# Performance work log

Hardware: AMD Instinct MI355X
Metric: run time of the kernel (lower is better)

The kernel has to match this reference:

```python
import jax, jax.numpy as jnp
import numpy as np


def _xavier(key, shape):
    fan_out, fan_in = shape[0], shape[1]
    lim = np.sqrt(6.0 / (fan_in + fan_out)).astype(np.float32)
    return jax.random.uniform(key, shape, jnp.float32, -lim, lim)


def setup_inputs() -> dict:
    key = jax.random.key(0)
    ks = jax.random.split(key, 28)
    B, D, G, ND = 16384, 32, 6, 8
    V_user, V_item, V_gender, V_age, V_occ, V_genre = 1000000, 100000, 2, 7, 21, 19
    H1, H2 = 128, 64
    deep_in = 6 * D + ND  # 200
    return {
        "user_id": jax.random.randint(ks[0], (B,), 0, V_user),
        "item_id": jax.random.randint(ks[1], (B,), 0, V_item),
        "user_gender": jax.random.randint(ks[2], (B,), 0, V_gender),
        "user_age": jax.random.randint(ks[3], (B,), 0, V_age),
        "user_occupation": jax.random.randint(ks[4], (B,), 0, V_occ),
        "item_genre_ids": jax.random.randint(ks[5], (B, G), 0, V_genre),
        "item_genre_mask": jax.random.randint(ks[6], (B, G), 0, 2).astype(jnp.float32),
        "dense_features": jax.random.normal(ks[7], (B, ND), jnp.float32),
        # first-order (1-dim) embedding tables
        "fo_user": _xavier(ks[8], (V_user, 1)),
        "fo_item": _xavier(ks[9], (V_item, 1)),
        "fo_gender": _xavier(ks[10], (V_gender, 1)),
        "fo_age": _xavier(ks[11], (V_age, 1)),
        "fo_occ": _xavier(ks[12], (V_occ, 1)),
        "fo_genre": _xavier(ks[13], (V_genre, 1)),
        # second-order / deep embedding tables
        "emb_user": _xavier(ks[14], (V_user, D)),
        "emb_item": _xavier(ks[15], (V_item, D)),
        "emb_gender": _xavier(ks[16], (V_gender, D)),
        "emb_age": _xavier(ks[17], (V_age, D)),
        "emb_occ": _xavier(ks[18], (V_occ, D)),
        "emb_genre": _xavier(ks[19], (V_genre, D)),
        # dense linear + deep MLP
        "dense_W": _xavier(ks[20], (1, ND)),
        "dense_b": jnp.zeros((1,), jnp.float32),
        "W1": _xavier(ks[21], (H1, deep_in)),
        "b1": jnp.zeros((H1,), jnp.float32),
        "W2": _xavier(ks[22], (H2, H1)),
        "b2": jnp.zeros((H2,), jnp.float32),
        "Wout": _xavier(ks[23], (1, H2)),
        "bout": jnp.zeros((1,), jnp.float32),
    }


def _pool(table, ids, mask):
    # masked mean-pool over the genre list axis
    e = table[ids]                       # [B, G, d]
    m = mask[..., None]                  # [B, G, 1]
    denom = jnp.clip(m.sum(axis=1), 1.0)  # [B, 1]
    return (e * m).sum(axis=1) / denom   # [B, d]


def reference(user_id, item_id, user_gender, user_age, user_occupation,
              item_genre_ids, item_genre_mask, dense_features,
              fo_user, fo_item, fo_gender, fo_age, fo_occ, fo_genre,
              emb_user, emb_item, emb_gender, emb_age, emb_occ, emb_genre,
              dense_W, dense_b, W1, b1, W2, b2, Wout, bout):
    # FM first order: sum of 1-dim gathers + pooled genre + dense linear -> [B,1]
    first = (fo_user[user_id] + fo_item[item_id] + fo_gender[user_gender]
             + fo_age[user_age] + fo_occ[user_occupation]
             + _pool(fo_genre, item_genre_ids, item_genre_mask)
             + dense_features @ dense_W.T + dense_b)
    # FM second order: stack field embeddings [B, 6, D]
    x = jnp.stack([emb_user[user_id], emb_item[item_id], emb_gender[user_gender],
                   emb_age[user_age], emb_occ[user_occupation],
                   _pool(emb_genre, item_genre_ids, item_genre_mask)], axis=1)
    s = x.sum(axis=1)                                   # [B, D]
    second = 0.5 * (s * s - (x * x).sum(axis=1)).sum(axis=1, keepdims=True)  # [B,1]
    # deep part (dropout is identity in eval mode)
    deep_in = jnp.concatenate([x.reshape(x.shape[0], -1), dense_features], axis=1)
    h = jax.nn.relu(deep_in @ W1.T + b1)
    h = jax.nn.relu(h @ W2.T + b2)
    deep = h @ Wout.T + bout                            # [B,1]
    return (first + second + deep).squeeze(1)           # [B]
```

## Files before the change

kernel.cpp:

```cpp
#include <hip/hip_runtime.h>


#define WAVES_PER_BLOCK 4
#define ROWS_PER_WAVE 8
#define ROWS_PER_BLOCK (WAVES_PER_BLOCK * ROWS_PER_WAVE)

__global__ __launch_bounds__(256) void deepfm_kernel(
    const int* __restrict__ user_id, const int* __restrict__ item_id,
    const int* __restrict__ gender_, const int* __restrict__ age_,
    const int* __restrict__ occ_, const int* __restrict__ genre_ids,
    const float* __restrict__ genre_mask, const float* __restrict__ dense,
    const float* __restrict__ fo_user, const float* __restrict__ fo_item,
    const float* __restrict__ fo_gender, const float* __restrict__ fo_age,
    const float* __restrict__ fo_occ, const float* __restrict__ fo_genre,
    const float* __restrict__ emb_user, const float* __restrict__ emb_item,
    const float* __restrict__ emb_gender, const float* __restrict__ emb_age,
    const float* __restrict__ emb_occ, const float* __restrict__ emb_genre,
    const float* __restrict__ dense_W, const float* __restrict__ dense_b,
    const float* __restrict__ W1, const float* __restrict__ b1,
    const float* __restrict__ W2, const float* __restrict__ b2,
    const float* __restrict__ Wout, const float* __restrict__ bout,
    float* __restrict__ out, int B)
{
    __shared__ float lds_di[WAVES_PER_BLOCK][ROWS_PER_WAVE][200];
    __shared__ float lds_rs[WAVES_PER_BLOCK][ROWS_PER_WAVE];

    const int tid = threadIdx.x;
    const int wid = tid >> 6;
    const int lane = tid & 63;
    const int rowBase = blockIdx.x * ROWS_PER_BLOCK + wid * ROWS_PER_WAVE;

    for (int r = 0; r < ROWS_PER_WAVE; ++r) {
        const int row = rowBase + r;
        if (row >= B) break;

        const int uid = user_id[row], iid = item_id[row];
        const int g = gender_[row], a = age_[row], o = occ_[row];

        int gid[6]; float mk[6]; float msum = 0.f;
        #pragma unroll
        for (int t = 0; t < 6; ++t) {
            gid[t] = genre_ids[row * 6 + t];
            mk[t]  = genre_mask[row * 6 + t];
            msum  += mk[t];
        }
        const float inv_den = 1.0f / fmaxf(msum, 1.0f);

        float pe_sum = 0.f, pe_sq = 0.f;
        {
            float v = (lane < 32) ? emb_user[(size_t)uid * 32 + lane]
                                  : emb_item[(size_t)iid * 32 + (lane - 32)];
            lds_di[wid][r][lane] = v;
            pe_sum += v; pe_sq += v * v;
        }
        {
            float v = (lane < 32) ? emb_gender[g * 32 + lane]
                                  : emb_age[a * 32 + (lane - 32)];
            lds_di[wid][r][64 + lane] = v;
            pe_sum += v; pe_sq += v * v;
        }
        {
            float v;
            if (lane < 32) {
                v = emb_occ[o * 32 + lane];
            } else {
                const int d = lane - 32;
                float s = 0.f;
                #pragma unroll
                for (int t = 0; t < 6; ++t) s += mk[t] * emb_genre[gid[t] * 32 + d];
                v = s * inv_den;
            }
            lds_di[wid][r][128 + lane] = v;
            pe_sum += v; pe_sq += v * v;
        }
        if (lane < 8) lds_di[wid][r][192 + lane] = dense[(size_t)row * 8 + lane];

        float s2 = pe_sum + __shfl_xor(pe_sum, 32);
        float ss = pe_sq  + __shfl_xor(pe_sq, 32);
        float t2 = 0.5f * (s2 * s2 - ss);
        #pragma unroll
        for (int off = 16; off >= 1; off >>= 1) t2 += __shfl_xor(t2, off);

        float fo = fo_user[uid] + fo_item[iid] + fo_gender[g] + fo_age[a] + fo_occ[o];
        float fg = 0.f;
        #pragma unroll
        for (int t = 0; t < 6; ++t) fg += mk[t] * fo_genre[gid[t]];
        fo += fg * inv_den;
        float dd = 0.f;
        #pragma unroll
        for (int j = 0; j < 8; ++j) dd += dense[(size_t)row * 8 + j] * dense_W[j];
        fo += dd + dense_b[0];

        if (lane == 0) lds_rs[wid][r] = fo + t2;
    }
    __syncthreads();

    float acc0[ROWS_PER_WAVE], acc1[ROWS_PER_WAVE];
    #pragma unroll
    for (int r = 0; r < ROWS_PER_WAVE; ++r) { acc0[r] = 0.f; acc1[r] = 0.f; }

    const float4* __restrict__ W1v = reinterpret_cast<const float4*>(W1);
    const float4* __restrict__ div_ = reinterpret_cast<const float4*>(&lds_di[wid][0][0]);

    for (int k4 = 0; k4 < 50; ++k4) {
        const float4 w0 = W1v[lane * 50 + k4];
        const float4 w1 = W1v[(lane + 64) * 50 + k4];
        #pragma unroll
        for (int r = 0; r < ROWS_PER_WAVE; ++r) {
            const float4 di = div_[r * 50 + k4];
            acc0[r] += w0.x * di.x + w0.y * di.y + w0.z * di.z + w0.w * di.w;
            acc1[r] += w1.x * di.x + w1.y * di.y + w1.z * di.z + w1.w * di.w;
        }
    }

    __syncthreads();
    float* __restrict__ h1b = &lds_di[wid][0][0];
    {
        const float bb0 = b1[lane], bb1 = b1[lane + 64];
        #pragma unroll
        for (int r = 0; r < ROWS_PER_WAVE; ++r) {
            h1b[r * 128 + lane]      = fmaxf(acc0[r] + bb0, 0.f);
            h1b[r * 128 + lane + 64] = fmaxf(acc1[r] + bb1, 0.f);
        }
    }
    __syncthreads();

    float acc2[ROWS_PER_WAVE];
    #pragma unroll
    for (int r = 0; r < ROWS_PER_WAVE; ++r) acc2[r] = 0.f;

    const float4* __restrict__ W2v = reinterpret_cast<const float4*>(W2);
    const float4* __restrict__ h1v = reinterpret_cast<const float4*>(h1b);

    for (int k4 = 0; k4 < 32; ++k4) {
        const float4 w = W2v[lane * 32 + k4];
        #pragma unroll
        for (int r = 0; r < ROWS_PER_WAVE; ++r) {
            const float4 h = h1v[r * 32 + k4];
            acc2[r] += w.x * h.x + w.y * h.y + w.z * h.z + w.w * h.w;
        }
    }

    const float wo = Wout[lane];
    const float bb2 = b2[lane];
    const float bo = bout[0];
    for (int r = 0; r < ROWS_PER_WAVE; ++r) {
        const int row = rowBase + r;
        const float h2 = fmaxf(acc2[r] + bb2, 0.f);
        float v = wo * h2;
        #pragma unroll
        for (int off = 32; off >= 1; off >>= 1) v += __shfl_xor(v, off);
        if (lane == 0 && row < B) out[row] = v + bo + lds_rs[wid][r];
    }
}

extern "C" void kernel_launch(void* const* d_in, const int* in_sizes, int n_in,
                              void* d_out, int out_size, void* d_ws, size_t ws_size,
                              hipStream_t stream) {
    const int B = in_sizes[0];
    const int grid = (B + ROWS_PER_BLOCK - 1) / ROWS_PER_BLOCK;
    deepfm_kernel<<<grid, 256, 0, stream>>>(
        (const int*)d_in[0],  (const int*)d_in[1],  (const int*)d_in[2],
        (const int*)d_in[3],  (const int*)d_in[4],  (const int*)d_in[5],
        (const float*)d_in[6],  (const float*)d_in[7],
        (const float*)d_in[8],  (const float*)d_in[9],  (const float*)d_in[10],
        (const float*)d_in[11], (const float*)d_in[12], (const float*)d_in[13],
        (const float*)d_in[14], (const float*)d_in[15], (const float*)d_in[16],
        (const float*)d_in[17], (const float*)d_in[18], (const float*)d_in[19],
        (const float*)d_in[20], (const float*)d_in[21],
        (const float*)d_in[22], (const float*)d_in[23],
        (const float*)d_in[24], (const float*)d_in[25],
        (const float*)d_in[26], (const float*)d_in[27],
        (float*)d_out, B);
}
```

Before: 271.0 us.

## Pre-pack MLP weights into coalesced float4 layout and batch index loads

Adds a small pre-kernel that repacks W1 and W2 into the workspace so that each lane's float4 weight load is contiguous across the wavefront, replacing strided row-major loads. Lane-to-output mapping for layer 1 changes to adjacent output pairs, with float2 bias and h1 stores. Index loads for all rows of a wave are now hoisted ahead of the gather loop and the loop is unrolled, which exposes more memory-level parallelism for the embedding gathers. The cost is an extra kernel launch each call and higher register pressure from the unrolled row loop.

```diff
diff --git a/kernel.cpp b/kernel.cpp
--- a/kernel.cpp
+++ b/kernel.cpp
@@ -4,6 +4,22 @@
 #define WAVES_PER_BLOCK 4
 #define ROWS_PER_WAVE 8
 #define ROWS_PER_BLOCK (WAVES_PER_BLOCK * ROWS_PER_WAVE)
+
+__global__ void pack_weights(const float* __restrict__ W1, const float* __restrict__ W2,
+                             float4* __restrict__ W1p, float4* __restrict__ W2p) {
+    const int idx = blockIdx.x * blockDim.x + threadIdx.x;
+    if (idx < 100 * 64) {
+        const int k2 = idx >> 6, l = idx & 63;
+        const int j0 = 2 * l, j1 = 2 * l + 1, k0 = 2 * k2, k1 = 2 * k2 + 1;
+        W1p[idx] = make_float4(W1[j0 * 200 + k0], W1[j1 * 200 + k0],
+                               W1[j0 * 200 + k1], W1[j1 * 200 + k1]);
+    }
+    if (idx < 32 * 64) {
+        const int k4 = idx >> 6, l = idx & 63;
+        const float* r = W2 + l * 128 + 4 * k4;
+        W2p[idx] = make_float4(r[0], r[1], r[2], r[3]);
+    }
+}
 
 __global__ __launch_bounds__(256) void deepfm_kernel(
     const int* __restrict__ user_id, const int* __restrict__ item_id,
@@ -17,8 +33,8 @@
     const float* __restrict__ emb_gender, const float* __restrict__ emb_age,
     const float* __restrict__ emb_occ, const float* __restrict__ emb_genre,
     const float* __restrict__ dense_W, const float* __restrict__ dense_b,
-    const float* __restrict__ W1, const float* __restrict__ b1,
-    const float* __restrict__ W2, const float* __restrict__ b2,
+    const float4* __restrict__ W1p, const float* __restrict__ b1,
+    const float4* __restrict__ W2p, const float* __restrict__ b2,
     const float* __restrict__ Wout, const float* __restrict__ bout,
     float* __restrict__ out, int B)
 {
@@ -30,12 +46,18 @@
     const int lane = tid & 63;
     const int rowBase = blockIdx.x * ROWS_PER_BLOCK + wid * ROWS_PER_WAVE;
 
+    int uid[ROWS_PER_WAVE], iid[ROWS_PER_WAVE], gg[ROWS_PER_WAVE],
+        aa[ROWS_PER_WAVE], oo[ROWS_PER_WAVE];
+    #pragma unroll
     for (int r = 0; r < ROWS_PER_WAVE; ++r) {
-        const int row = rowBase + r;
-        if (row >= B) break;
-
-        const int uid = user_id[row], iid = item_id[row];
-        const int g = gender_[row], a = age_[row], o = occ_[row];
+        int row = rowBase + r; if (row >= B) row = B - 1;
+        uid[r] = user_id[row]; iid[r] = item_id[row];
+        gg[r] = gender_[row];  aa[r] = age_[row];  oo[r] = occ_[row];
+    }
+
+    #pragma unroll
+    for (int r = 0; r < ROWS_PER_WAVE; ++r) {
+        int row = rowBase + r; if (row >= B) row = B - 1;
 
         int gid[6]; float mk[6]; float msum = 0.f;
         #pragma unroll
@@ -48,21 +70,21 @@
 
         float pe_sum = 0.f, pe_sq = 0.f;
         {
-            float v = (lane < 32) ? emb_user[(size_t)uid * 32 + lane]
-                                  : emb_item[(size_t)iid * 32 + (lane - 32)];
+            float v = (lane < 32) ? emb_user[(size_t)uid[r] * 32 + lane]
+                                  : emb_item[(size_t)iid[r] * 32 + (lane - 32)];
             lds_di[wid][r][lane] = v;
             pe_sum += v; pe_sq += v * v;
         }
         {
-            float v = (lane < 32) ? emb_gender[g * 32 + lane]
-                                  : emb_age[a * 32 + (lane - 32)];
+            float v = (lane < 32) ? emb_gender[gg[r] * 32 + lane]
+                                  : emb_age[aa[r] * 32 + (lane - 32)];
             lds_di[wid][r][64 + lane] = v;
             pe_sum += v; pe_sq += v * v;
         }
         {
             float v;
             if (lane < 32) {
-                v = emb_occ[o * 32 + lane];
+                v = emb_occ[oo[r] * 32 + lane];
             } else {
                 const int d = lane - 32;
                 float s = 0.f;
@@ -81,7 +103,8 @@
         #pragma unroll
         for (int off = 16; off >= 1; off >>= 1) t2 += __shfl_xor(t2, off);
 
-        float fo = fo_user[uid] + fo_item[iid] + fo_gender[g] + fo_age[a] + fo_occ[o];
+        float fo = fo_user[uid[r]] + fo_item[iid[r]] + fo_gender[gg[r]]
+                 + fo_age[aa[r]] + fo_occ[oo[r]];
         float fg = 0.f;
         #pragma unroll
         for (int t = 0; t < 6; ++t) fg += mk[t] * fo_genre[gid[t]];
@@ -99,28 +122,27 @@
     #pragma unroll
     for (int r = 0; r < ROWS_PER_WAVE; ++r) { acc0[r] = 0.f; acc1[r] = 0.f; }
 
-    const float4* __restrict__ W1v = reinterpret_cast<const float4*>(W1);
     const float4* __restrict__ div_ = reinterpret_cast<const float4*>(&lds_di[wid][0][0]);
 
     for (int k4 = 0; k4 < 50; ++k4) {
-        const float4 w0 = W1v[lane * 50 + k4];
-        const float4 w1 = W1v[(lane + 64) * 50 + k4];
+        const float4 w0 = W1p[(2 * k4) * 64 + lane];
+        const float4 w1 = W1p[(2 * k4 + 1) * 64 + lane];
         #pragma unroll
         for (int r = 0; r < ROWS_PER_WAVE; ++r) {
-            const float4 di = div_[r * 50 + k4];
-            acc0[r] += w0.x * di.x + w0.y * di.y + w0.z * di.z + w0.w * di.w;
-            acc1[r] += w1.x * di.x + w1.y * di.y + w1.z * di.z + w1.w * di.w;
+            const float4 a = div_[r * 50 + k4];
+            acc0[r] += w0.x * a.x + w0.z * a.y + w1.x * a.z + w1.z * a.w;
+            acc1[r] += w0.y * a.x + w0.w * a.y + w1.y * a.z + w1.w * a.w;
         }
     }
 
     __syncthreads();
     float* __restrict__ h1b = &lds_di[wid][0][0];
     {
-        const float bb0 = b1[lane], bb1 = b1[lane + 64];
+        const float2 bb = *reinterpret_cast<const float2*>(b1 + 2 * lane);
         #pragma unroll
         for (int r = 0; r < ROWS_PER_WAVE; ++r) {
-            h1b[r * 128 + lane]      = fmaxf(acc0[r] + bb0, 0.f);
-            h1b[r * 128 + lane + 64] = fmaxf(acc1[r] + bb1, 0.f);
+            reinterpret_cast<float2*>(h1b)[r * 64 + lane] =
+                make_float2(fmaxf(acc0[r] + bb.x, 0.f), fmaxf(acc1[r] + bb.y, 0.f));
         }
     }
     __syncthreads();
@@ -129,11 +151,10 @@
     #pragma unroll
     for (int r = 0; r < ROWS_PER_WAVE; ++r) acc2[r] = 0.f;
 
-    const float4* __restrict__ W2v = reinterpret_cast<const float4*>(W2);
     const float4* __restrict__ h1v = reinterpret_cast<const float4*>(h1b);
 
     for (int k4 = 0; k4 < 32; ++k4) {
-        const float4 w = W2v[lane * 32 + k4];
+        const float4 w = W2p[k4 * 64 + lane];
         #pragma unroll
         for (int r = 0; r < ROWS_PER_WAVE; ++r) {
             const float4 h = h1v[r * 32 + k4];
@@ -158,6 +179,13 @@
                               void* d_out, int out_size, void* d_ws, size_t ws_size,
                               hipStream_t stream) {
     const int B = in_sizes[0];
+
+    float4* W1p = reinterpret_cast<float4*>(d_ws);
+    float4* W2p = reinterpret_cast<float4*>((char*)d_ws + 102400);
+
+    pack_weights<<<25, 256, 0, stream>>>(
+        (const float*)d_in[22], (const float*)d_in[24], W1p, W2p);
+
     const int grid = (B + ROWS_PER_BLOCK - 1) / ROWS_PER_BLOCK;
     deepfm_kernel<<<grid, 256, 0, stream>>>(
         (const int*)d_in[0],  (const int*)d_in[1],  (const int*)d_in[2],
@@ -168,8 +196,8 @@
         (const float*)d_in[14], (const float*)d_in[15], (const float*)d_in[16],
         (const float*)d_in[17], (const float*)d_in[18], (const float*)d_in[19],
         (const float*)d_in[20], (const float*)d_in[21],
-        (const float*)d_in[22], (const float*)d_in[23],
-        (const float*)d_in[24], (const float*)d_in[25],
+        W1p, (const float*)d_in[23],
+        W2p, (const float*)d_in[25],
         (const float*)d_in[26], (const float*)d_in[27],
         (float*)d_out, B);
 }
```

Result: no change. 266.1 us (-1.8%).
